# Kernel optimization log

Hardware: AMD Instinct MI355X
Metric: run time of the kernel (lower is better)

## Reference

```python
import jax, jax.numpy as jnp
import numpy as np

D_MODEL = 2048
N_HEADS = 16
D_HEAD = D_MODEL // N_HEADS  # 128
RANK = 32


def _orthogonal(key, rows, cols, dtype=jnp.float32):
    # mimic torch orthogonal init via QR
    a = jax.random.normal(key, (max(rows, cols), min(rows, cols)), dtype=jnp.float32)
    q, r = jnp.linalg.qr(a)
    q = q * jnp.sign(jnp.diagonal(r))
    if rows < cols:
        q = q.T
    return q.astype(dtype)


def setup_inputs() -> dict:
    key = jax.random.key(0)
    ks = jax.random.split(key, 8)
    B, T = 2, 2048
    x = jax.random.normal(ks[0], (B, T, D_MODEL), dtype=jnp.float32)
    s = 1.0 / np.sqrt(D_MODEL)
    Wq = jax.random.uniform(ks[1], (D_MODEL, D_MODEL), minval=-s, maxval=s, dtype=jnp.float32)
    Wk = jax.random.uniform(ks[2], (D_MODEL, D_MODEL), minval=-s, maxval=s, dtype=jnp.float32)
    Wv = jax.random.uniform(ks[3], (D_MODEL, D_MODEL), minval=-s, maxval=s, dtype=jnp.float32)
    Wo = jax.random.uniform(ks[4], (D_MODEL, D_MODEL), minval=-s, maxval=s, dtype=jnp.float32)
    # vein projector: project d_head -> rank, reconstruct rank -> d_head (orthogonal init)
    Wdown = _orthogonal(ks[5], D_HEAD, RANK)   # [d_head, r]
    Wup = _orthogonal(ks[6], RANK, D_HEAD)     # [r, d_head]
    return {"x": x, "Wq": Wq, "Wk": Wk, "Wv": Wv, "Wo": Wo, "Wdown": Wdown, "Wup": Wup}


def reference(x, Wq, Wk, Wv, Wo, Wdown, Wup):
    B, T, D = x.shape
    H, dh, r = N_HEADS, D_HEAD, RANK
    scale = 1.0 / np.sqrt(r)

    def heads(y):  # [B,T,D] -> [B,H,T,dh]
        return y.reshape(B, T, H, dh).transpose(0, 2, 1, 3)

    q = heads(x @ Wq.T)
    k = heads(x @ Wk.T)
    v = heads(x @ Wv.T)

    # project into vein (rank) space: [B,H,T,r]
    q_r = jnp.einsum('bhtd,dr->bhtr', q, Wdown)
    k_r = jnp.einsum('bhtd,dr->bhtr', k, Wdown)
    v_r = jnp.einsum('bhtd,dr->bhtr', v, Wdown)

    scores = jnp.einsum('bhqr,bhkr->bhqk', q_r, k_r) * scale  # [B,H,T,T]
    attn = jax.nn.softmax(scores, axis=-1)
    y_r = jnp.einsum('bhqk,bhkr->bhqr', attn, v_r)            # [B,H,T,r]
    y = jnp.einsum('bhtr,rd->bhtd', y_r, Wup)                  # reconstruct [B,H,T,dh]
    y = y.transpose(0, 2, 1, 3).reshape(B, T, D)
    out = y @ Wo.T
    return out
```

## Files before the change

kernel.cpp:

```cpp
#include <hip/hip_runtime.h>
#include <cstdint>
#include <cstddef>

typedef __bf16 bf16;
typedef __attribute__((ext_vector_type(8))) __bf16 bf16x8;
typedef __attribute__((ext_vector_type(4))) float f32x4;
typedef unsigned int u32;

#define D_MODEL 2048
#define QSCALE  0.17677669529663687f

__device__ inline void async_load16(const void* gp, void* lp) {
  __builtin_amdgcn_global_load_lds(
      (const __attribute__((address_space(1))) u32*)gp,
      (__attribute__((address_space(3))) u32*)lp, 16, 0, 0);
}

__global__ __launch_bounds__(256) void cvt_k(const float* __restrict__ x,
                                             bf16* __restrict__ xb) {
  const int i = (blockIdx.x * 256 + threadIdx.x) * 8;
  float4 a = *(const float4*)(x + i);
  float4 b = *(const float4*)(x + i + 4);
  bf16x8 o;
  o[0] = (bf16)a.x; o[1] = (bf16)a.y; o[2] = (bf16)a.z; o[3] = (bf16)a.w;
  o[4] = (bf16)b.x; o[5] = (bf16)b.y; o[6] = (bf16)b.z; o[7] = (bf16)b.w;
  *(bf16x8*)(xb + i) = o;
}

__global__ __launch_bounds__(256) void fold_qkv_k(
    const float* __restrict__ Wq, const float* __restrict__ Wk,
    const float* __restrict__ Wv, const float* __restrict__ Wdown,
    bf16* __restrict__ EffT) {
  __shared__ float wd[128][32];
  const int t = threadIdx.x;
  for (int i = t; i < 128 * 32; i += 256)
    ((float*)wd)[i] = Wdown[i];
  __syncthreads();
  const int mh = blockIdx.x;
  const float* W = (mh < 16) ? Wq : ((mh < 32) ? Wk : Wv);
  const int hrow = (mh & 15) * 128;
  const int d = blockIdx.y * 128 + (t & 127);
  const int rh = (t >> 7) * 16;
  float acc[16];
#pragma unroll
  for (int j = 0; j < 16; ++j) acc[j] = 0.f;
#pragma unroll 4
  for (int k = 0; k < 128; ++k) {
    float w = W[(size_t)(hrow + k) * D_MODEL + d];
    const float* wr = &wd[k][rh];
#pragma unroll
    for (int j = 0; j < 16; ++j) acc[j] += w * wr[j];
  }
  bf16* outp = EffT + (size_t)(mh * 32 + rh) * D_MODEL + d;
#pragma unroll
  for (int j = 0; j < 16; ++j) outp[(size_t)j * D_MODEL] = (bf16)acc[j];
}

__global__ __launch_bounds__(256) void fold_o_k(
    const bf16* __restrict__ Wob, const float* __restrict__ Wup,
    bf16* __restrict__ WoEffT) {
  __shared__ __align__(16) bf16 As_[128 * 128];
  __shared__ __align__(16) bf16 Bs_[32 * 128];
  const int t = threadIdx.x, wave = t >> 6, lane = t & 63;
  const int quad = lane >> 4, lc = lane & 15;
  const int d0 = blockIdx.x * 128, h = blockIdx.y;
#pragma unroll
  for (int a = 0; a < 8; ++a) {
    int r0 = wave * 32 + a * 4;
    int row = r0 + (lane >> 4);
    int g = (lane & 15) ^ (row & 15);
    async_load16(Wob + (size_t)(d0 + row) * 2048 + h * 128 + g * 8,
                 As_ + r0 * 128);
  }
  {
    int row = t >> 3;
    int c0 = (t & 7) * 2;
    const float* src = Wup + row * 128 + c0 * 8;
    float4 f0 = ((const float4*)src)[0], f1 = ((const float4*)src)[1];
    float4 f2 = ((const float4*)src)[2], f3 = ((const float4*)src)[3];
    bf16x8 b0, b1;
    b0[0] = (bf16)f0.x; b0[1] = (bf16)f0.y; b0[2] = (bf16)f0.z; b0[3] = (bf16)f0.w;
    b0[4] = (bf16)f1.x; b0[5] = (bf16)f1.y; b0[6] = (bf16)f1.z; b0[7] = (bf16)f1.w;
    b1[0] = (bf16)f2.x; b1[1] = (bf16)f2.y; b1[2] = (bf16)f2.z; b1[3] = (bf16)f2.w;
    b1[4] = (bf16)f3.x; b1[5] = (bf16)f3.y; b1[6] = (bf16)f3.z; b1[7] = (bf16)f3.w;
    *(bf16x8*)(Bs_ + row * 128 + ((c0 ^ (row & 15)) * 8)) = b0;
    *(bf16x8*)(Bs_ + row * 128 + (((c0 + 1) ^ (row & 15)) * 8)) = b1;
  }
  __syncthreads();
  f32x4 acc[2][2] = {};
  const int wm = wave * 32;
#pragma unroll
  for (int kc = 0; kc < 4; ++kc) {
    bf16x8 af[2], bfr[2];
#pragma unroll
    for (int mi = 0; mi < 2; ++mi) {
      int m = wm + mi * 16 + lc;
      af[mi] = *(const bf16x8*)(As_ + m * 128 + (((kc * 4 + quad) ^ (m & 15)) * 8));
    }
#pragma unroll
    for (int ni = 0; ni < 2; ++ni) {
      int n = ni * 16 + lc;
      bfr[ni] = *(const bf16x8*)(Bs_ + n * 128 + (((kc * 4 + quad) ^ (n & 15)) * 8));
    }
#pragma unroll
    for (int mi = 0; mi < 2; ++mi)
#pragma unroll
      for (int ni = 0; ni < 2; ++ni)
        acc[mi][ni] = __builtin_amdgcn_mfma_f32_16x16x32_bf16(
            af[mi], bfr[ni], acc[mi][ni], 0, 0, 0);
  }
#pragma unroll
  for (int mi = 0; mi < 2; ++mi)
#pragma unroll
    for (int ni = 0; ni < 2; ++ni)
#pragma unroll
      for (int reg = 0; reg < 4; ++reg)
        WoEffT[(size_t)(d0 + wm + mi * 16 + quad * 4 + reg) * 512 + h * 32 +
               ni * 16 + lc] = (bf16)acc[mi][ni][reg];
}

template <int EPI>
__global__ __launch_bounds__(256) void gemm_bt_k(
    const bf16* __restrict__ A, const bf16* __restrict__ Bt,
    void* __restrict__ Cv, int M, int N, int K) {
  __shared__ __align__(16) bf16 As[2][64 * 64];
  __shared__ __align__(16) bf16 Bs[2][128 * 64];
  const int t = threadIdx.x, wave = t >> 6, lane = t & 63;
  const int quad = lane >> 4, lc = lane & 15;
  const size_t m0 = (size_t)blockIdx.x * 64;
  const size_t n0 = (size_t)blockIdx.y * 128;
  const int wm = (wave >> 1) * 32, wn = (wave & 1) * 64;
  const int sr = lane >> 3, ss = lane & 7;
  const bf16* Aga[2]; int Aoff[2];
#pragma unroll
  for (int a = 0; a < 2; ++a) {
    int row = wave * 16 + a * 8 + sr;
    Aga[a] = A + (m0 + row) * (size_t)K + (ss ^ (row & 7)) * 8;
    Aoff[a] = (wave * 16 + a * 8) * 64;
  }
  const bf16* Bga[4]; int Boff[4];
#pragma unroll
  for (int a = 0; a < 4; ++a) {
    int row = wave * 32 + a * 8 + sr;
    Bga[a] = Bt + (n0 + row) * (size_t)K + (ss ^ (row & 7)) * 8;
    Boff[a] = (wave * 32 + a * 8) * 64;
  }
  f32x4 acc[2][4] = {};
  const int NIT = K >> 6;
#pragma unroll
  for (int a = 0; a < 2; ++a) async_load16(Aga[a], &As[0][Aoff[a]]);
#pragma unroll
  for (int a = 0; a < 4; ++a) async_load16(Bga[a], &Bs[0][Boff[a]]);
  __syncthreads();
  for (int it = 0; it < NIT; ++it) {
    const int cur = it & 1;
    if (it + 1 < NIT) {
      const int k0 = (it + 1) * 64;
#pragma unroll
      for (int a = 0; a < 2; ++a) async_load16(Aga[a] + k0, &As[1 - cur][Aoff[a]]);
#pragma unroll
      for (int a = 0; a < 4; ++a) async_load16(Bga[a] + k0, &Bs[1 - cur][Boff[a]]);
    }
    const bf16* Asb = As[cur];
    const bf16* Bsb = Bs[cur];
#pragma unroll
    for (int kc = 0; kc < 2; ++kc) {
      bf16x8 af[2], bfr[4];
#pragma unroll
      for (int mi = 0; mi < 2; ++mi) {
        int m = wm + mi * 16 + lc;
        af[mi] = *(const bf16x8*)(Asb + m * 64 + (((kc * 4 + quad) ^ (m & 7)) * 8));
      }
#pragma unroll
      for (int ni = 0; ni < 4; ++ni) {
        int n = wn + ni * 16 + lc;
        bfr[ni] = *(const bf16x8*)(Bsb + n * 64 + (((kc * 4 + quad) ^ (n & 7)) * 8));
      }
#pragma unroll
      for (int mi = 0; mi < 2; ++mi)
#pragma unroll
        for (int ni = 0; ni < 4; ++ni)
          acc[mi][ni] = __builtin_amdgcn_mfma_f32_16x16x32_bf16(
              af[mi], bfr[ni], acc[mi][ni], 0, 0, 0);
    }
    __syncthreads();
  }

  if (EPI == 0) {
    float* C = (float*)Cv;
#pragma unroll
    for (int mi = 0; mi < 2; ++mi)
#pragma unroll
      for (int ni = 0; ni < 4; ++ni) {
        size_t row = m0 + wm + mi * 16 + quad * 4;
        size_t col = n0 + wn + ni * 16 + lc;
#pragma unroll
        for (int reg = 0; reg < 4; ++reg)
          C[(row + reg) * (size_t)N + col] = acc[mi][ni][reg];
      }
  } else {
    bf16* C = (bf16*)Cv;
#pragma unroll
    for (int mi = 0; mi < 2; ++mi)
#pragma unroll
      for (int ni = 0; ni < 4; ++ni) {
        int n = (int)n0 + wn + ni * 16 + lc;
        int mat = n >> 9, hh = (n >> 5) & 15, r = n & 31;
        float sc = (mat == 0) ? QSCALE : 1.0f;
        int trow = (int)m0 + wm + mi * 16 + quad * 4;
#pragma unroll
        for (int reg = 0; reg < 4; ++reg) {
          int tr = trow + reg;
          int b = tr >> 11, tl = tr & 2047;
          size_t off = ((((size_t)(b * 16 + hh)) * 3 + mat) * 2048 + tl) * 32 + r;
          C[off] = (bf16)(acc[mi][ni][reg] * sc);
        }
      }
  }
}

__global__ __launch_bounds__(256) void attn_k(const bf16* __restrict__ QKVr,
                                              bf16* __restrict__ Yr) {
  const int bh = blockIdx.x, qb = blockIdx.y;
  const size_t base = (size_t)bh * 3 * 2048 * 32;
  const bf16* Q  = QKVr + base;
  const bf16* Kr = Q + 2048 * 32;
  const bf16* Vr = Kr + 2048 * 32;
  __shared__ __align__(16) bf16 Ks[2][128 * 32];
  __shared__ __align__(16) bf16 Vt[2][32 * 128];
  __shared__ __align__(16) bf16 Ps[4][16 * 128];
  const int t = threadIdx.x, wave = t >> 6, lane = t & 63;
  const int quad = lane >> 4, lc = lane & 15;
  const int qrow = qb * 64 + wave * 16 + lc;
  const bf16x8 qf = *(const bf16x8*)(Q + (size_t)qrow * 32 + quad * 8);
  f32x4 o0 = {}, o1 = {};
  float ls[4] = {0.f, 0.f, 0.f, 0.f};
  const int krow = wave * 16 + (lane >> 2);
  const bf16* Kg = Kr + (size_t)krow * 32 + ((lane & 3) ^ ((krow >> 1) & 3)) * 8;
  const int vkk = t >> 2, vrs = (t & 3) * 8;
  bf16* pw = Ps[wave];

  bf16x8 va, vb;
  async_load16(Kg, &Ks[0][wave * 16 * 32]);
  async_load16(Kg + (size_t)64 * 32, &Ks[0][(64 + wave * 16) * 32]);
  va = *(const bf16x8*)(Vr + (size_t)vkk * 32 + vrs);
  vb = *(const bf16x8*)(Vr + (size_t)(64 + vkk) * 32 + vrs);
  {
    int ca = vkk >> 3, cb = 8 + (vkk >> 3);
#pragma unroll
    for (int j = 0; j < 8; ++j) {
      int r = vrs + j;
      Vt[0][r * 128 + ((ca ^ (r & 15)) * 8) + (vkk & 7)] = va[j];
      Vt[0][r * 128 + ((cb ^ (r & 15)) * 8) + (vkk & 7)] = vb[j];
    }
  }
  __syncthreads();

  for (int it = 0; it < 16; ++it) {
    const int kt = it * 128, cur = it & 1;
    bf16x8 na, nb;
    if (it < 15) {
      async_load16(Kg + (size_t)(kt + 128) * 32, &Ks[1 - cur][wave * 16 * 32]);
      async_load16(Kg + (size_t)(kt + 192) * 32, &Ks[1 - cur][(64 + wave * 16) * 32]);
      na = *(const bf16x8*)(Vr + (size_t)(kt + 128 + vkk) * 32 + vrs);
      nb = *(const bf16x8*)(Vr + (size_t)(kt + 192 + vkk) * 32 + vrs);
    }
    const bf16* ksb = Ks[cur];
    f32x4 s[8];
#pragma unroll
    for (int ni = 0; ni < 8; ++ni) {
      int n = ni * 16 + lc;
      bf16x8 kf = *(const bf16x8*)(ksb + n * 32 + ((quad ^ ((n >> 1) & 3)) * 8));
      f32x4 z = {0.f, 0.f, 0.f, 0.f};
      s[ni] = __builtin_amdgcn_mfma_f32_16x16x32_bf16(qf, kf, z, 0, 0, 0);
    }
#pragma unroll
    for (int ni = 0; ni < 8; ++ni)
#pragma unroll
      for (int reg = 0; reg < 4; ++reg) {
        float e = __expf(s[ni][reg]);
        s[ni][reg] = e;
        ls[reg] += e;
      }
#pragma unroll
    for (int ni = 0; ni < 8; ++ni) {
      int col = ni * 16 + lc;
      int cb2 = col >> 3;
#pragma unroll
      for (int reg = 0; reg < 4; ++reg) {
        int prow = quad * 4 + reg;
        pw[prow * 128 + ((cb2 ^ prow) * 8) + (col & 7)] = (bf16)s[ni][reg];
      }
    }
    const bf16* vtb = Vt[cur];
#pragma unroll
    for (int kc = 0; kc < 4; ++kc) {
      int ch = kc * 4 + quad;
      bf16x8 pf = *(const bf16x8*)(pw + lc * 128 + ((ch ^ lc) * 8));
      bf16x8 v0 = *(const bf16x8*)(vtb + lc * 128 + ((ch ^ lc) * 8));
      bf16x8 v1 = *(const bf16x8*)(vtb + (16 + lc) * 128 + ((ch ^ lc) * 8));
      o0 = __builtin_amdgcn_mfma_f32_16x16x32_bf16(pf, v0, o0, 0, 0, 0);
      o1 = __builtin_amdgcn_mfma_f32_16x16x32_bf16(pf, v1, o1, 0, 0, 0);
    }
    if (it < 15) {
      int ca = vkk >> 3, cb = 8 + (vkk >> 3);
#pragma unroll
      for (int j = 0; j < 8; ++j) {
        int r = vrs + j;
        Vt[1 - cur][r * 128 + ((ca ^ (r & 15)) * 8) + (vkk & 7)] = na[j];
        Vt[1 - cur][r * 128 + ((cb ^ (r & 15)) * 8) + (vkk & 7)] = nb[j];
      }
    }
    __syncthreads();
  }
  const int b = bh >> 4, h = bh & 15;
#pragma unroll
  for (int reg = 0; reg < 4; ++reg) {
    float v = ls[reg];
    v += __shfl_xor(v, 1);
    v += __shfl_xor(v, 2);
    v += __shfl_xor(v, 4);
    v += __shfl_xor(v, 8);
    float inv = 1.0f / v;
    size_t row = (size_t)b * 2048 + qb * 64 + wave * 16 + quad * 4 + reg;
    Yr[row * 512 + h * 32 + lc]      = (bf16)(o0[reg] * inv);
    Yr[row * 512 + h * 32 + 16 + lc] = (bf16)(o1[reg] * inv);
  }
}

extern "C" void kernel_launch(void* const* d_in, const int* in_sizes, int n_in,
                              void* d_out, int out_size, void* d_ws, size_t ws_size,
                              hipStream_t stream) {
  const float* x     = (const float*)d_in[0];
  const float* Wq    = (const float*)d_in[1];
  const float* Wk    = (const float*)d_in[2];
  const float* Wv    = (const float*)d_in[3];
  const float* Wo    = (const float*)d_in[4];
  const float* Wdown = (const float*)d_in[5];
  const float* Wup   = (const float*)d_in[6];
  float* out = (float*)d_out;

  char* ws = (char*)d_ws;
  bf16* EffT   = (bf16*)(ws);
  bf16* WoEffT = (bf16*)(ws + 6291456);
  bf16* QKVr   = (bf16*)(ws + 8388608);
  bf16* Wob    = (bf16*)(ws + 8388608);
  bf16* Yrb    = (bf16*)(ws + 20971520);
  bf16* xb     = (bf16*)(ws + 25165824);

  cvt_k<<<dim3(4096), dim3(256), 0, stream>>>(x, xb);
  cvt_k<<<dim3(2048), dim3(256), 0, stream>>>(Wo, Wob);
  fold_qkv_k<<<dim3(48, 16), dim3(256), 0, stream>>>(Wq, Wk, Wv, Wdown, EffT);
  fold_o_k<<<dim3(16, 16), dim3(256), 0, stream>>>(Wob, Wup, WoEffT);
  gemm_bt_k<1><<<dim3(64, 12), dim3(256), 0, stream>>>(xb, EffT, QKVr,
                                                       4096, 1536, 2048);
  attn_k<<<dim3(32, 32), dim3(256), 0, stream>>>(QKVr, Yrb);
  gemm_bt_k<0><<<dim3(64, 16), dim3(256), 0, stream>>>(Yrb, WoEffT, out,
                                                       4096, 2048, 512);
}
```

Measured before the change: 270.1 us.

## Enlarge GEMM and attention tiles, transpose score MFMA for vectorized P stores

The GEMM tile grows from 64x128 to 128x128, so each wave computes a 64x64 sub-tile and every B tile loaded into shared memory is reused over twice as many rows. The attention kernel now handles 32 query rows per wave (128 per block), so each K/V tile staged in LDS is reused twice as often. The score MFMA operands are swapped so each lane holds consecutive keys for one query, which allows packed bf16x4 writes of P and packed bf16x2 V-transpose stores, with the row sums reduced by cross-lane shuffles at the end. The cost is more registers and LDS per block and half as many blocks, which may lower occupancy and leave CUs idle on smaller grids.

```diff
diff --git a/kernel.cpp b/kernel.cpp
--- a/kernel.cpp
+++ b/kernel.cpp
@@ -4,6 +4,8 @@
 
 typedef __bf16 bf16;
 typedef __attribute__((ext_vector_type(8))) __bf16 bf16x8;
+typedef __attribute__((ext_vector_type(4))) __bf16 bf16x4;
+typedef __attribute__((ext_vector_type(2))) __bf16 bf16x2;
 typedef __attribute__((ext_vector_type(4))) float f32x4;
 typedef unsigned int u32;
 
@@ -123,51 +125,47 @@
 __global__ __launch_bounds__(256) void gemm_bt_k(
     const bf16* __restrict__ A, const bf16* __restrict__ Bt,
     void* __restrict__ Cv, int M, int N, int K) {
-  __shared__ __align__(16) bf16 As[2][64 * 64];
+  __shared__ __align__(16) bf16 As[2][128 * 64];
   __shared__ __align__(16) bf16 Bs[2][128 * 64];
   const int t = threadIdx.x, wave = t >> 6, lane = t & 63;
   const int quad = lane >> 4, lc = lane & 15;
-  const size_t m0 = (size_t)blockIdx.x * 64;
+  const size_t m0 = (size_t)blockIdx.x * 128;
   const size_t n0 = (size_t)blockIdx.y * 128;
-  const int wm = (wave >> 1) * 32, wn = (wave & 1) * 64;
+  const int wm = (wave >> 1) * 64, wn = (wave & 1) * 64;
   const int sr = lane >> 3, ss = lane & 7;
-  const bf16* Aga[2]; int Aoff[2];
-#pragma unroll
-  for (int a = 0; a < 2; ++a) {
-    int row = wave * 16 + a * 8 + sr;
-    Aga[a] = A + (m0 + row) * (size_t)K + (ss ^ (row & 7)) * 8;
-    Aoff[a] = (wave * 16 + a * 8) * 64;
-  }
-  const bf16* Bga[4]; int Boff[4];
+  const bf16* Aga[4]; const bf16* Bga[4]; int Loff[4];
 #pragma unroll
   for (int a = 0; a < 4; ++a) {
     int row = wave * 32 + a * 8 + sr;
+    Aga[a] = A + (m0 + row) * (size_t)K + (ss ^ (row & 7)) * 8;
     Bga[a] = Bt + (n0 + row) * (size_t)K + (ss ^ (row & 7)) * 8;
-    Boff[a] = (wave * 32 + a * 8) * 64;
-  }
-  f32x4 acc[2][4] = {};
+    Loff[a] = (wave * 32 + a * 8) * 64;
+  }
+  f32x4 acc[4][4] = {};
   const int NIT = K >> 6;
 #pragma unroll
-  for (int a = 0; a < 2; ++a) async_load16(Aga[a], &As[0][Aoff[a]]);
-#pragma unroll
-  for (int a = 0; a < 4; ++a) async_load16(Bga[a], &Bs[0][Boff[a]]);
+  for (int a = 0; a < 4; ++a) {
+    async_load16(Aga[a], &As[0][Loff[a]]);
+    async_load16(Bga[a], &Bs[0][Loff[a]]);
+  }
   __syncthreads();
   for (int it = 0; it < NIT; ++it) {
     const int cur = it & 1;
     if (it + 1 < NIT) {
       const int k0 = (it + 1) * 64;
 #pragma unroll
-      for (int a = 0; a < 2; ++a) async_load16(Aga[a] + k0, &As[1 - cur][Aoff[a]]);
-#pragma unroll
-      for (int a = 0; a < 4; ++a) async_load16(Bga[a] + k0, &Bs[1 - cur][Boff[a]]);
+      for (int a = 0; a < 4; ++a) {
+        async_load16(Aga[a] + k0, &As[1 - cur][Loff[a]]);
+        async_load16(Bga[a] + k0, &Bs[1 - cur][Loff[a]]);
+      }
     }
     const bf16* Asb = As[cur];
     const bf16* Bsb = Bs[cur];
 #pragma unroll
     for (int kc = 0; kc < 2; ++kc) {
-      bf16x8 af[2], bfr[4];
-#pragma unroll
-      for (int mi = 0; mi < 2; ++mi) {
+      bf16x8 af[4], bfr[4];
+#pragma unroll
+      for (int mi = 0; mi < 4; ++mi) {
         int m = wm + mi * 16 + lc;
         af[mi] = *(const bf16x8*)(Asb + m * 64 + (((kc * 4 + quad) ^ (m & 7)) * 8));
       }
@@ -177,7 +175,7 @@
         bfr[ni] = *(const bf16x8*)(Bsb + n * 64 + (((kc * 4 + quad) ^ (n & 7)) * 8));
       }
 #pragma unroll
-      for (int mi = 0; mi < 2; ++mi)
+      for (int mi = 0; mi < 4; ++mi)
 #pragma unroll
         for (int ni = 0; ni < 4; ++ni)
           acc[mi][ni] = __builtin_amdgcn_mfma_f32_16x16x32_bf16(
@@ -189,7 +187,7 @@
   if (EPI == 0) {
     float* C = (float*)Cv;
 #pragma unroll
-    for (int mi = 0; mi < 2; ++mi)
+    for (int mi = 0; mi < 4; ++mi)
 #pragma unroll
       for (int ni = 0; ni < 4; ++ni) {
         size_t row = m0 + wm + mi * 16 + quad * 4;
@@ -201,7 +199,7 @@
   } else {
     bf16* C = (bf16*)Cv;
 #pragma unroll
-    for (int mi = 0; mi < 2; ++mi)
+    for (int mi = 0; mi < 4; ++mi)
 #pragma unroll
       for (int ni = 0; ni < 4; ++ni) {
         int n = (int)n0 + wn + ni * 16 + lc;
@@ -228,30 +226,30 @@
   const bf16* Vr = Kr + 2048 * 32;
   __shared__ __align__(16) bf16 Ks[2][128 * 32];
   __shared__ __align__(16) bf16 Vt[2][32 * 128];
-  __shared__ __align__(16) bf16 Ps[4][16 * 128];
+  __shared__ __align__(16) bf16 Ps[4 * 32 * 128];
   const int t = threadIdx.x, wave = t >> 6, lane = t & 63;
   const int quad = lane >> 4, lc = lane & 15;
-  const int qrow = qb * 64 + wave * 16 + lc;
-  const bf16x8 qf = *(const bf16x8*)(Q + (size_t)qrow * 32 + quad * 8);
-  f32x4 o0 = {}, o1 = {};
-  float ls[4] = {0.f, 0.f, 0.f, 0.f};
+  const int qbase = qb * 128 + wave * 32;
+  const bf16x8 qf0 = *(const bf16x8*)(Q + (size_t)(qbase + lc) * 32 + quad * 8);
+  const bf16x8 qf1 = *(const bf16x8*)(Q + (size_t)(qbase + 16 + lc) * 32 + quad * 8);
+  f32x4 o00 = {}, o01 = {}, o10 = {}, o11 = {};
+  float ls0 = 0.f, ls1 = 0.f;
   const int krow = wave * 16 + (lane >> 2);
   const bf16* Kg = Kr + (size_t)krow * 32 + ((lane & 3) ^ ((krow >> 1) & 3)) * 8;
-  const int vkk = t >> 2, vrs = (t & 3) * 8;
-  bf16* pw = Ps[wave];
-
-  bf16x8 va, vb;
+  const int va_ = t >> 2;
+  const int vrs = (t & 3) * 8;
+  bf16* pw = Ps + wave * 32 * 128;
+
   async_load16(Kg, &Ks[0][wave * 16 * 32]);
   async_load16(Kg + (size_t)64 * 32, &Ks[0][(64 + wave * 16) * 32]);
-  va = *(const bf16x8*)(Vr + (size_t)vkk * 32 + vrs);
-  vb = *(const bf16x8*)(Vr + (size_t)(64 + vkk) * 32 + vrs);
   {
-    int ca = vkk >> 3, cb = 8 + (vkk >> 3);
+    bf16x8 va = *(const bf16x8*)(Vr + (size_t)(2 * va_) * 32 + vrs);
+    bf16x8 vb = *(const bf16x8*)(Vr + (size_t)(2 * va_ + 1) * 32 + vrs);
 #pragma unroll
     for (int j = 0; j < 8; ++j) {
       int r = vrs + j;
-      Vt[0][r * 128 + ((ca ^ (r & 15)) * 8) + (vkk & 7)] = va[j];
-      Vt[0][r * 128 + ((cb ^ (r & 15)) * 8) + (vkk & 7)] = vb[j];
+      bf16x2 p = {va[j], vb[j]};
+      *(bf16x2*)(Vt[0] + r * 128 + (((va_ >> 2) ^ (r & 15)) * 8) + (va_ & 3) * 2) = p;
     }
   }
   __syncthreads();
@@ -262,69 +260,63 @@
     if (it < 15) {
       async_load16(Kg + (size_t)(kt + 128) * 32, &Ks[1 - cur][wave * 16 * 32]);
       async_load16(Kg + (size_t)(kt + 192) * 32, &Ks[1 - cur][(64 + wave * 16) * 32]);
-      na = *(const bf16x8*)(Vr + (size_t)(kt + 128 + vkk) * 32 + vrs);
-      nb = *(const bf16x8*)(Vr + (size_t)(kt + 192 + vkk) * 32 + vrs);
+      na = *(const bf16x8*)(Vr + (size_t)(kt + 128 + 2 * va_) * 32 + vrs);
+      nb = *(const bf16x8*)(Vr + (size_t)(kt + 128 + 2 * va_ + 1) * 32 + vrs);
     }
     const bf16* ksb = Ks[cur];
-    f32x4 s[8];
 #pragma unroll
     for (int ni = 0; ni < 8; ++ni) {
       int n = ni * 16 + lc;
       bf16x8 kf = *(const bf16x8*)(ksb + n * 32 + ((quad ^ ((n >> 1) & 3)) * 8));
       f32x4 z = {0.f, 0.f, 0.f, 0.f};
-      s[ni] = __builtin_amdgcn_mfma_f32_16x16x32_bf16(qf, kf, z, 0, 0, 0);
-    }
-#pragma unroll
-    for (int ni = 0; ni < 8; ++ni)
+      f32x4 s0 = __builtin_amdgcn_mfma_f32_16x16x32_bf16(kf, qf0, z, 0, 0, 0);
+      f32x4 s1 = __builtin_amdgcn_mfma_f32_16x16x32_bf16(kf, qf1, z, 0, 0, 0);
+      bf16x4 p0, p1;
 #pragma unroll
       for (int reg = 0; reg < 4; ++reg) {
-        float e = __expf(s[ni][reg]);
-        s[ni][reg] = e;
-        ls[reg] += e;
-      }
-#pragma unroll
-    for (int ni = 0; ni < 8; ++ni) {
-      int col = ni * 16 + lc;
-      int cb2 = col >> 3;
-#pragma unroll
-      for (int reg = 0; reg < 4; ++reg) {
-        int prow = quad * 4 + reg;
-        pw[prow * 128 + ((cb2 ^ prow) * 8) + (col & 7)] = (bf16)s[ni][reg];
-      }
+        float e0 = __expf(s0[reg]); ls0 += e0; p0[reg] = (bf16)e0;
+        float e1 = __expf(s1[reg]); ls1 += e1; p1[reg] = (bf16)e1;
+      }
+      int off = (((2 * ni + (quad >> 1)) ^ lc) * 8) + (quad & 1) * 4;
+      *(bf16x4*)(pw + lc * 128 + off) = p0;
+      *(bf16x4*)(pw + (16 + lc) * 128 + off) = p1;
     }
     const bf16* vtb = Vt[cur];
 #pragma unroll
     for (int kc = 0; kc < 4; ++kc) {
-      int ch = kc * 4 + quad;
-      bf16x8 pf = *(const bf16x8*)(pw + lc * 128 + ((ch ^ lc) * 8));
-      bf16x8 v0 = *(const bf16x8*)(vtb + lc * 128 + ((ch ^ lc) * 8));
-      bf16x8 v1 = *(const bf16x8*)(vtb + (16 + lc) * 128 + ((ch ^ lc) * 8));
-      o0 = __builtin_amdgcn_mfma_f32_16x16x32_bf16(pf, v0, o0, 0, 0, 0);
-      o1 = __builtin_amdgcn_mfma_f32_16x16x32_bf16(pf, v1, o1, 0, 0, 0);
+      int co = ((kc * 4 + quad) ^ lc) * 8;
+      bf16x8 pf0 = *(const bf16x8*)(pw + lc * 128 + co);
+      bf16x8 pf1 = *(const bf16x8*)(pw + (16 + lc) * 128 + co);
+      bf16x8 v0 = *(const bf16x8*)(vtb + lc * 128 + co);
+      bf16x8 v1 = *(const bf16x8*)(vtb + (16 + lc) * 128 + co);
+      o00 = __builtin_amdgcn_mfma_f32_16x16x32_bf16(pf0, v0, o00, 0, 0, 0);
+      o01 = __builtin_amdgcn_mfma_f32_16x16x32_bf16(pf0, v1, o01, 0, 0, 0);
+      o10 = __builtin_amdgcn_mfma_f32_16x16x32_bf16(pf1, v0, o10, 0, 0, 0);
+      o11 = __builtin_amdgcn_mfma_f32_16x16x32_bf16(pf1, v1, o11, 0, 0, 0);
     }
     if (it < 15) {
-      int ca = vkk >> 3, cb = 8 + (vkk >> 3);
 #pragma unroll
       for (int j = 0; j < 8; ++j) {
         int r = vrs + j;
-        Vt[1 - cur][r * 128 + ((ca ^ (r & 15)) * 8) + (vkk & 7)] = na[j];
-        Vt[1 - cur][r * 128 + ((cb ^ (r & 15)) * 8) + (vkk & 7)] = nb[j];
+        bf16x2 p = {na[j], nb[j]};
+        *(bf16x2*)(Vt[1 - cur] + r * 128 + (((va_ >> 2) ^ (r & 15)) * 8) + (va_ & 3) * 2) = p;
       }
     }
     __syncthreads();
   }
+  ls0 += __shfl_xor(ls0, 16); ls0 += __shfl_xor(ls0, 32);
+  ls1 += __shfl_xor(ls1, 16); ls1 += __shfl_xor(ls1, 32);
   const int b = bh >> 4, h = bh & 15;
 #pragma unroll
   for (int reg = 0; reg < 4; ++reg) {
-    float v = ls[reg];
-    v += __shfl_xor(v, 1);
-    v += __shfl_xor(v, 2);
-    v += __shfl_xor(v, 4);
-    v += __shfl_xor(v, 8);
-    float inv = 1.0f / v;
-    size_t row = (size_t)b * 2048 + qb * 64 + wave * 16 + quad * 4 + reg;
-    Yr[row * 512 + h * 32 + lc]      = (bf16)(o0[reg] * inv);
-    Yr[row * 512 + h * 32 + 16 + lc] = (bf16)(o1[reg] * inv);
+    float i0 = 1.0f / __shfl(ls0, quad * 4 + reg);
+    float i1 = 1.0f / __shfl(ls1, quad * 4 + reg);
+    size_t r0 = (size_t)b * 2048 + qbase + quad * 4 + reg;
+    size_t r1 = r0 + 16;
+    Yr[r0 * 512 + h * 32 + lc]      = (bf16)(o00[reg] * i0);
+    Yr[r0 * 512 + h * 32 + 16 + lc] = (bf16)(o01[reg] * i0);
+    Yr[r1 * 512 + h * 32 + lc]      = (bf16)(o10[reg] * i1);
+    Yr[r1 * 512 + h * 32 + 16 + lc] = (bf16)(o11[reg] * i1);
   }
 }
 
@@ -352,9 +344,9 @@
   cvt_k<<<dim3(2048), dim3(256), 0, stream>>>(Wo, Wob);
   fold_qkv_k<<<dim3(48, 16), dim3(256), 0, stream>>>(Wq, Wk, Wv, Wdown, EffT);
   fold_o_k<<<dim3(16, 16), dim3(256), 0, stream>>>(Wob, Wup, WoEffT);
-  gemm_bt_k<1><<<dim3(64, 12), dim3(256), 0, stream>>>(xb, EffT, QKVr,
+  gemm_bt_k<1><<<dim3(32, 12), dim3(256), 0, stream>>>(xb, EffT, QKVr,
                                                        4096, 1536, 2048);
-  attn_k<<<dim3(32, 32), dim3(256), 0, stream>>>(QKVr, Yrb);
-  gemm_bt_k<0><<<dim3(64, 16), dim3(256), 0, stream>>>(Yrb, WoEffT, out,
+  attn_k<<<dim3(32, 16), dim3(256), 0, stream>>>(QKVr, Yrb);
+  gemm_bt_k<0><<<dim3(32, 16), dim3(256), 0, stream>>>(Yrb, WoEffT, out,
                                                        4096, 2048, 512);
 }
```

Result: faster. 256.4 us (-5.1%).
